# Performance work log

Measured on AMD Instinct MI355X. Metric: run time of the kernel, lower is better.

## Reference

```python
import jax, jax.numpy as jnp
import numpy as np

X_MIN, X_MAX = -2.0, 2.0


def _pchip_slopes_uniform(y, h):
    # y: [..., K], uniform knot spacing h. Fritsch-Carlson / PCHIP slopes.
    delta = (y[..., 1:] - y[..., :-1]) / h            # [..., K-1]
    dp, dn = delta[..., :-1], delta[..., 1:]          # [..., K-2]
    same_sign = dp * dn > 0
    d_mid = jnp.where(same_sign, 2.0 * dp * dn / (dp + dn + 1e-12), 0.0)

    def _fix_endpoint(d_end, delta0, delta1):
        d_end = jnp.where(d_end * delta0 <= 0, 0.0, d_end)
        d_end = jnp.where((delta0 * delta1 < 0) & (jnp.abs(d_end) > 3.0 * jnp.abs(delta0)),
                          3.0 * delta0, d_end)
        return d_end

    d0 = _fix_endpoint((3.0 * delta[..., 0] - delta[..., 1]) / 2.0, delta[..., 0], delta[..., 1])
    dN = _fix_endpoint((3.0 * delta[..., -1] - delta[..., -2]) / 2.0, delta[..., -1], delta[..., -2])
    return jnp.concatenate([d0[..., None], d_mid, dN[..., None]], axis=-1)


def setup_inputs() -> dict:
    key = jax.random.key(0)
    k1, k2 = jax.random.split(key)
    B, O, D, K = 8192, 64, 64, 64
    x = jax.random.normal(k1, (B, D), dtype=jnp.float32)
    coeffs = 0.01 * jax.random.normal(k2, (O, D, K), dtype=jnp.float32)
    bias = jnp.zeros((O,), dtype=jnp.float32)
    return {"x": x, "coeffs": coeffs, "bias": bias}


def reference(x, coeffs, bias):
    # x: [B, D]; coeffs: [O, D, K]; bias: [O] -> out: [B, O]
    O, D, K = coeffs.shape
    h = (X_MAX - X_MIN) / (K - 1)
    slopes = _pchip_slopes_uniform(coeffs, h)          # [O, D, K]

    t = (x - X_MIN) / h                                # [B, D]
    idx = jnp.clip(jnp.floor(t).astype(jnp.int32), 0, K - 2)
    u = (t - idx)[None]                                # [1, B, D]

    darange = jnp.arange(D)[None, :]                   # broadcasts with idx [B, D]
    y0 = coeffs[:, darange, idx]                       # [O, B, D]
    y1 = coeffs[:, darange, idx + 1]
    d0 = slopes[:, darange, idx]
    d1 = slopes[:, darange, idx + 1]

    u2 = u * u
    u3 = u2 * u
    h00 = 2.0 * u3 - 3.0 * u2 + 1.0
    h10 = u3 - 2.0 * u2 + u
    h01 = -2.0 * u3 + 3.0 * u2
    h11 = u3 - u2
    interp = h00 * y0 + h10 * (h * d0) + h01 * y1 + h11 * (h * d1)  # [O, B, D]

    # linear extrapolation outside [X_MIN, X_MAX]
    left = coeffs[:, :, 0][:, None, :] + slopes[:, :, 0][:, None, :] * (x - X_MIN)[None]
    right = coeffs[:, :, -1][:, None, :] + slopes[:, :, -1][:, None, :] * (x - X_MAX)[None]
    interp = jnp.where((x < X_MIN)[None], left, interp)
    interp = jnp.where((x > X_MAX)[None], right, interp)

    out = interp.sum(axis=-1).T + bias[None, :]        # [B, O]
    return out
```

## Files before the change

### kernel.cpp

```cpp
#include <hip/hip_runtime.h>
#include <hip/hip_fp16.h>
#include <stdint.h>


typedef _Float16 half2v __attribute__((ext_vector_type(2)));

#if defined(__has_builtin)
#if __has_builtin(__builtin_amdgcn_fdot2)
#define HAS_FDOT2 1
#endif
#endif

__device__ __forceinline__ uint32_t h16(float f) {
    return (uint32_t)__half_as_ushort(__float2half(f));
}

__device__ __forceinline__ float dot2acc(uint32_t a_bits, uint32_t b_bits, float acc) {
    half2v a = __builtin_bit_cast(half2v, a_bits);
    half2v b = __builtin_bit_cast(half2v, b_bits);
#ifdef HAS_FDOT2
    return __builtin_amdgcn_fdot2(a, b, acc, false);
#else
    return acc + (float)a.x * (float)b.x + (float)a.y * (float)b.y;
#endif
}

__global__ void build_table(const float* __restrict__ coeffs, uint2* __restrict__ T,
                            const float* __restrict__ bias, float* __restrict__ out) {
    const float hf = 4.0f / 63.0f;
    const float inv_hf = 63.0f / 4.0f;
    int d  = blockIdx.x >> 2;
    int ob = (blockIdx.x & 3) << 4;
    __shared__ float Y[16][65];
    int t = threadIdx.x;
    {
        int ol = t >> 4;
        int k4 = (t & 15) << 2;
        const float* src = coeffs + (size_t)(ob + ol) * 4096 + d * 64 + k4;
        float4 v = *(const float4*)src;
        Y[ol][k4 + 0] = v.x; Y[ol][k4 + 1] = v.y;
        Y[ol][k4 + 2] = v.z; Y[ol][k4 + 3] = v.w;
    }
    {
        float bv = bias[t & 63];
        int g = blockIdx.x * 2048 + t;
        #pragma unroll
        for (int i = 0; i < 8; ++i) out[g + i * 256] = bv;
    }
    __syncthreads();
    for (int c = t; c < 1024; c += 256) {
        int ol = c & 15;
        int i  = c >> 4;
        const float* Yr = Y[ol];
        auto delt = [&](int k) -> float { return (Yr[k + 1] - Yr[k]) * inv_hf; };
        auto endslope = [&](float a, float b) -> float {
            float de = (3.0f * a - b) * 0.5f;
            de = (de * a <= 0.0f) ? 0.0f : de;
            de = ((a * b < 0.0f) && (fabsf(de) > 3.0f * fabsf(a))) ? 3.0f * a : de;
            return de;
        };
        auto slope = [&](int k) -> float {
            if (k == 0)  return endslope(delt(0), delt(1));
            if (k == 63) return endslope(delt(62), delt(61));
            float dp = delt(k - 1), dn = delt(k);
            return (dp * dn > 0.0f) ? (2.0f * dp * dn) / (dp + dn + 1e-12f) : 0.0f;
        };
        uint2 pk;
        if (i < 63) {
            float y0 = Yr[i], y1 = Yr[i + 1];
            float di = slope(i), dj = slope(i + 1);
            float c0 = y0;
            float c1 = hf * di;
            float c2 = 3.0f * (y1 - y0) - hf * (2.0f * di + dj);
            float c3 = 2.0f * (y0 - y1) + hf * (di + dj);
            pk.x = (h16(c1) << 16) | h16(c0);
            pk.y = (h16(c3) << 16) | h16(c2);
        } else {
            float yN = Yr[63];
            float dN = slope(63);
            pk.x = (h16(hf * dN) << 16) | h16(yN);
            pk.y = 0u;
        }
        T[(size_t)d * 4096 + i * 64 + (ob + ol)] = pk;
    }
}

__global__ void __launch_bounds__(512) kan_main(const float* __restrict__ x,
                                                const char* __restrict__ Tb,
                                                float* __restrict__ out) {
    __shared__ uint4 TLs[2][2048];
    __shared__ uint4 REC[256][8];

    const int t     = threadIdx.x;
    const int lane  = t & 63;
    const int wv    = t >> 6;
    const int p     = blockIdx.x & 7;
    const int btile = blockIdx.x >> 3;
    const int dg    = p << 3;
    const int bbase = btile << 8;
    char* TL = (char*)TLs;

    {
        const char* src = Tb + ((size_t)dg << 15);
        #pragma unroll
        for (int r = 0; r < 4; ++r) {
            __builtin_amdgcn_global_load_lds(
                (const uint32_t*)(src + t * 16 + r * 8192),
                (uint32_t*)(TL + t * 16 + r * 8192), 16, 0, 0);
        }
    }

    #pragma unroll
    for (int k = 0; k < 4; ++k) {
        int r  = t + (k << 9);
        int bl = r >> 3;
        int dl = r & 7;
        float xv = x[(bbase + bl) * 64 + dg + dl];
        float tt = (xv + 2.0f) * 15.75f;
        int i = (int)floorf(tt);
        i = i < 0 ? 0 : (i > 62 ? 62 : i);
        float u = tt - (float)i;
        float w1, w2, w3; uint32_t off;
        if (xv < -2.0f)      { w1 = tt;          w2 = 0.f;    w3 = 0.f;     off = 0u; }
        else if (xv > 2.0f)  { w1 = tt - 63.0f;  w2 = 0.f;    w3 = 0.f;     off = 63u << 9; }
        else                 { w1 = u;           w2 = u * u;  w3 = w2 * u;  off = (uint32_t)i << 9; }
        half2v wa; wa.x = (_Float16)1.0f; wa.y = (_Float16)w1;
        half2v wb; wb.x = (_Float16)w2;   wb.y = (_Float16)w3;
        REC[bl][dl] = make_uint4(__builtin_bit_cast(uint32_t, wa),
                                 __builtin_bit_cast(uint32_t, wb), off, 0u);
    }
    __syncthreads();

    float acc[32];
    #pragma unroll
    for (int j = 0; j < 32; ++j) acc[j] = 0.0f;

    const int laneoff = lane << 3;
    const int blbase  = wv << 5;
    for (int c = 0; c < 8; ++c) {
        if (c < 7) {
            const char* src = Tb + ((size_t)(dg + c + 1) << 15);
            char* dst = TL + ((c + 1) & 1) * 32768;
            #pragma unroll
            for (int r = 0; r < 4; ++r) {
                __builtin_amdgcn_global_load_lds(
                    (const uint32_t*)(src + t * 16 + r * 8192),
                    (uint32_t*)(dst + t * 16 + r * 8192), 16, 0, 0);
            }
        }
        const char* TLc = TL + (c & 1) * 32768;
        #pragma unroll
        for (int j = 0; j < 32; ++j) {
            uint4 r0 = REC[blbase + j][c];
            uint2 q0 = *(const uint2*)(TLc + r0.z + laneoff);
            acc[j] = dot2acc(r0.x, q0.x, acc[j]);
            acc[j] = dot2acc(r0.y, q0.y, acc[j]);
        }
        __syncthreads();
    }

    float* dst = out + (size_t)(bbase + blbase) * 64 + lane;
    #pragma unroll
    for (int j = 0; j < 32; ++j) {
        atomicAdd(dst + j * 64, acc[j]);
    }
}

extern "C" void kernel_launch(void* const* d_in, const int* in_sizes, int n_in,
                              void* d_out, int out_size, void* d_ws, size_t ws_size,
                              hipStream_t stream) {
    const float* x      = (const float*)d_in[0];
    const float* coeffs = (const float*)d_in[1];
    const float* bias   = (const float*)d_in[2];
    float* out = (float*)d_out;

    uint2* T = (uint2*)d_ws;
    build_table<<<dim3(256), dim3(256), 0, stream>>>(coeffs, T, bias, out);
    kan_main<<<dim3(256), dim3(512), 0, stream>>>(x, (const char*)T, out);
}
```

Before: 87.24 us.

## Keep per-sample weights in registers via readlane, use 1024-thread blocks

Drops the shared-memory REC staging of per-(batch,dim) Hermite weights and offsets. Each lane now computes one record and the wave broadcasts it with readlane. Blocks grow to 1024 threads, each covering 128 batch rows, and the grid doubles to 512, so each wave owns 8 rows instead of 32. This removes the LDS record traffic and the register-heavy 32-wide accumulator, and raises occupancy. In exchange the coefficient table is loaded twice as often per batch row and there are more output atomics per block.

```diff
diff --git a/kernel.cpp b/kernel.cpp
--- a/kernel.cpp
+++ b/kernel.cpp
@@ -85,37 +85,22 @@
     }
 }
 
-__global__ void __launch_bounds__(512) kan_main(const float* __restrict__ x,
-                                                const char* __restrict__ Tb,
-                                                float* __restrict__ out) {
-    __shared__ uint4 TLs[2][2048];
-    __shared__ uint4 REC[256][8];
+__global__ void __launch_bounds__(1024, 8) kan_main(const float* __restrict__ x,
+                                                    const char* __restrict__ Tb,
+                                                    float* __restrict__ out) {
+    __shared__ char BUF[2][32768];
 
     const int t     = threadIdx.x;
     const int lane  = t & 63;
     const int wv    = t >> 6;
-    const int p     = blockIdx.x & 7;
+    const int group = blockIdx.x & 7;
     const int btile = blockIdx.x >> 3;
-    const int dg    = p << 3;
-    const int bbase = btile << 8;
-    char* TL = (char*)TLs;
+    const int dg    = group << 3;
+    const int bw    = (btile << 7) + (wv << 3);
 
+    uint32_t wa_bits, wb_bits, off_bits;
     {
-        const char* src = Tb + ((size_t)dg << 15);
-        #pragma unroll
-        for (int r = 0; r < 4; ++r) {
-            __builtin_amdgcn_global_load_lds(
-                (const uint32_t*)(src + t * 16 + r * 8192),
-                (uint32_t*)(TL + t * 16 + r * 8192), 16, 0, 0);
-        }
-    }
-
-    #pragma unroll
-    for (int k = 0; k < 4; ++k) {
-        int r  = t + (k << 9);
-        int bl = r >> 3;
-        int dl = r & 7;
-        float xv = x[(bbase + bl) * 64 + dg + dl];
+        float xv = x[(bw + (lane & 7)) * 64 + dg + (lane >> 3)];
         float tt = (xv + 2.0f) * 15.75f;
         int i = (int)floorf(tt);
         i = i < 0 ? 0 : (i > 62 ? 62 : i);
@@ -126,43 +111,55 @@
         else                 { w1 = u;           w2 = u * u;  w3 = w2 * u;  off = (uint32_t)i << 9; }
         half2v wa; wa.x = (_Float16)1.0f; wa.y = (_Float16)w1;
         half2v wb; wb.x = (_Float16)w2;   wb.y = (_Float16)w3;
-        REC[bl][dl] = make_uint4(__builtin_bit_cast(uint32_t, wa),
-                                 __builtin_bit_cast(uint32_t, wb), off, 0u);
+        wa_bits  = __builtin_bit_cast(uint32_t, wa);
+        wb_bits  = __builtin_bit_cast(uint32_t, wb);
+        off_bits = off;
+    }
+
+    {
+        const char* src = Tb + ((size_t)dg << 15);
+        #pragma unroll
+        for (int r = 0; r < 2; ++r) {
+            __builtin_amdgcn_global_load_lds(
+                (const uint32_t*)(src + t * 16 + r * 16384),
+                (uint32_t*)(&BUF[0][0] + t * 16 + r * 16384), 16, 0, 0);
+        }
     }
     __syncthreads();
 
-    float acc[32];
+    float acc[8];
     #pragma unroll
-    for (int j = 0; j < 32; ++j) acc[j] = 0.0f;
+    for (int j = 0; j < 8; ++j) acc[j] = 0.0f;
 
     const int laneoff = lane << 3;
-    const int blbase  = wv << 5;
     for (int c = 0; c < 8; ++c) {
         if (c < 7) {
             const char* src = Tb + ((size_t)(dg + c + 1) << 15);
-            char* dst = TL + ((c + 1) & 1) * 32768;
+            char* dst = &BUF[(c + 1) & 1][0];
             #pragma unroll
-            for (int r = 0; r < 4; ++r) {
+            for (int r = 0; r < 2; ++r) {
                 __builtin_amdgcn_global_load_lds(
-                    (const uint32_t*)(src + t * 16 + r * 8192),
-                    (uint32_t*)(dst + t * 16 + r * 8192), 16, 0, 0);
+                    (const uint32_t*)(src + t * 16 + r * 16384),
+                    (uint32_t*)(dst + t * 16 + r * 16384), 16, 0, 0);
             }
         }
-        const char* TLc = TL + (c & 1) * 32768;
+        const char* bufc = &BUF[c & 1][0];
+        int cl = c << 3;
         #pragma unroll
-        for (int j = 0; j < 32; ++j) {
-            uint4 r0 = REC[blbase + j][c];
-            uint2 q0 = *(const uint2*)(TLc + r0.z + laneoff);
-            acc[j] = dot2acc(r0.x, q0.x, acc[j]);
-            acc[j] = dot2acc(r0.y, q0.y, acc[j]);
+        for (int j = 0; j < 8; ++j) {
+            uint32_t qa  = (uint32_t)__builtin_amdgcn_readlane((int)wa_bits,  cl + j);
+            uint32_t qb  = (uint32_t)__builtin_amdgcn_readlane((int)wb_bits,  cl + j);
+            uint32_t off = (uint32_t)__builtin_amdgcn_readlane((int)off_bits, cl + j);
+            uint2 q = *(const uint2*)(bufc + off + laneoff);
+            acc[j] = dot2acc(qa, q.x, acc[j]);
+            acc[j] = dot2acc(qb, q.y, acc[j]);
         }
         __syncthreads();
     }
 
-    float* dst = out + (size_t)(bbase + blbase) * 64 + lane;
     #pragma unroll
-    for (int j = 0; j < 32; ++j) {
-        atomicAdd(dst + j * 64, acc[j]);
+    for (int j = 0; j < 8; ++j) {
+        atomicAdd(out + (size_t)(bw + j) * 64 + lane, acc[j]);
     }
 }
 
@@ -176,5 +173,5 @@
 
     uint2* T = (uint2*)d_ws;
     build_table<<<dim3(256), dim3(256), 0, stream>>>(coeffs, T, bias, out);
-    kan_main<<<dim3(256), dim3(512), 0, stream>>>(x, (const char*)T, out);
+    kan_main<<<dim3(512), dim3(1024), 0, stream>>>(x, (const char*)T, out);
 }
```

Measured after the change: 107.2 us. +22.9%, slower.
